# Optimization experiments

Measured on AMD Instinct MI355X. Metric: run time of the kernel, lower is better.

The kernel has to match this reference:

```python
import jax, jax.numpy as jnp
import numpy as np

B, S, D = 4, 2048, 1024
H = 16
HD = D // H  # 64
ROPE_BASE = 10000.0


def _rope_cache(seq_len, dim, dtype=jnp.float32):
    inv_freq = 1.0 / (ROPE_BASE ** (jnp.arange(0, dim, 2, dtype=jnp.float32) / dim))
    t = jnp.arange(seq_len, dtype=jnp.float32)
    freqs = jnp.outer(t, inv_freq)            # [S, dim/2]
    emb = jnp.concatenate([freqs, freqs], -1)  # [S, dim]
    return jnp.cos(emb).astype(dtype), jnp.sin(emb).astype(dtype)


def _rotate_half(x):
    x1, x2 = jnp.split(x, 2, axis=-1)
    return jnp.concatenate([-x2, x1], axis=-1)


def setup_inputs() -> dict:
    key = jax.random.key(0)
    k1, k2, k3 = jax.random.split(key, 3)
    x = jax.random.normal(k1, (B, S, D), dtype=jnp.float32)
    attention_mask = jnp.ones((B, S), dtype=jnp.int32)
    # torch nn.Linear weight is [out, in]; we store [in, out] for x @ W
    w_qkv = jax.random.normal(k2, (D, 3 * D), dtype=jnp.float32) * (1.0 / np.sqrt(D))
    w_out = jax.random.normal(k3, (D, D), dtype=jnp.float32) * (1.0 / np.sqrt(D))
    return {"x": x, "attention_mask": attention_mask, "w_qkv": w_qkv, "w_out": w_out}


def reference(x, attention_mask, w_qkv, w_out):
    b, s, d = x.shape
    qkv = x @ w_qkv                                  # [B,S,3D]
    qkv = qkv.reshape(b, s, 3, H, HD)
    q, k, v = [jnp.transpose(qkv[:, :, i], (0, 2, 1, 3)) for i in range(3)]  # [B,H,S,HD]
    cos, sin = _rope_cache(s, HD, x.dtype)           # [S,HD]
    cos = cos[None, None]                            # [1,1,S,HD]
    sin = sin[None, None]
    q = q * cos + _rotate_half(q) * sin
    k = k * cos + _rotate_half(k) * sin
    scale = 1.0 / np.sqrt(HD)
    scores = jnp.einsum("bhqd,bhkd->bhqk", q, k) * scale  # [B,H,S,S]
    causal = jnp.triu(jnp.ones((s, s), dtype=bool), k=1)
    neg_inf = jnp.finfo(scores.dtype).min
    scores = jnp.where(causal[None, None], -jnp.inf, scores)
    pad = (attention_mask == 0)[:, None, None, :]    # [B,1,1,S]
    scores = jnp.where(pad, -jnp.inf, scores)
    attn = jax.nn.softmax(scores, axis=-1)
    out = jnp.einsum("bhqk,bhkd->bhqd", attn, v)     # [B,H,S,HD]
    out = jnp.transpose(out, (0, 2, 1, 3)).reshape(b, s, d)
    return out @ w_out
```

## Files before the change

### kernel.cpp

```cpp
#include <hip/hip_runtime.h>

#define BQ 4
#define SQ 2048
#define DQ 1024
#define HQ 16
#define BHQ 64

typedef __attribute__((ext_vector_type(8))) short short8;
typedef __attribute__((ext_vector_type(4))) float f32x4;
typedef __attribute__((ext_vector_type(16))) float f32x16;
typedef __attribute__((ext_vector_type(2))) unsigned int u32x2;
typedef unsigned short u16;
typedef unsigned int u32;
typedef unsigned long long u64;

__device__ __forceinline__ u16 f2bf(float f) {
  u32 u = __float_as_uint(f);
  u32 r = u + 0x7fffu + ((u >> 16) & 1u);
  return (u16)(r >> 16);
}
__device__ __forceinline__ float bf2f(u16 h) {
  return __uint_as_float(((u32)h) << 16);
}

__device__ __forceinline__ u32 pkbf(float lo, float hi_) {
  u32 r;
  asm("v_cvt_pk_bf16_f32 %0, %1, %2" : "=v"(r) : "v"(lo), "v"(hi_));
  return r;
}
__device__ __forceinline__ float fexp2(float x) {
  float r;
  asm("v_exp_f32 %0, %1" : "=v"(r) : "v"(x));
  return r;
}
__device__ __forceinline__ float xmax32(float x) { return fmaxf(x, __shfl_xor(x, 32)); }
__device__ __forceinline__ float xsum32(float x) { return x + __shfl_xor(x, 32); }
__device__ __forceinline__ u32 xword(u32 send) { return (u32)__shfl_xor((int)send, 32); }

__device__ __forceinline__ void gload_lds16(const void* g, void* l) {
  __builtin_amdgcn_global_load_lds(
      (const __attribute__((address_space(1))) u32*)(unsigned long long)g,
      (__attribute__((address_space(3))) u32*)(u32)(unsigned long long)l,
      16, 0, 0);
}

__device__ __forceinline__ void transpose_body(const float* __restrict__ in, u16* __restrict__ out,
                                               int R, int C, int bx, int by, int tid) {
  __shared__ float t[32][33];
  int c0 = bx * 32, r0 = by * 32;
  int tx = tid & 31, ty = tid >> 5;
  for (int rr = ty; rr < 32; rr += 8)
    t[rr][tx] = in[(size_t)(r0 + rr) * C + c0 + tx];
  __syncthreads();
  for (int rr = ty; rr < 32; rr += 8)
    out[(size_t)(c0 + rr) * R + r0 + tx] = f2bf(t[tx][rr]);
}

__global__ __launch_bounds__(256) void k_prep(const float* __restrict__ x, u16* __restrict__ xb,
                                              const float* __restrict__ wqkv, u16* __restrict__ wqkvT,
                                              const float* __restrict__ wout, u16* __restrict__ woutT,
                                              float* __restrict__ tab, const int* __restrict__ mask,
                                              u64* __restrict__ mbits) {
  int bid = blockIdx.x, tid = threadIdx.x;
  if (bid < 8192) {
    int i = bid * 256 + tid;
    float4 v = ((const float4*)x)[i];
    ushort4 o;
    o.x = f2bf(v.x); o.y = f2bf(v.y); o.z = f2bf(v.z); o.w = f2bf(v.w);
    ((ushort4*)xb)[i] = o;
  } else if (bid < 11264) {
    int t = bid - 8192;
    transpose_body(wqkv, wqkvT, 1024, 3072, t % 96, t / 96, tid);
  } else if (bid < 12288) {
    int t = bid - 11264;
    transpose_body(wout, woutT, 1024, 1024, t % 32, t / 32, tid);
  } else if (bid < 12544) {
    int i = (bid - 12288) * 256 + tid;
    int s = i >> 5, dp = i & 31;
    float invf = expf(-0.28782313662425576f * (float)dp);
    float ang = (float)s * invf;
    tab[i * 2] = cosf(ang);
    tab[i * 2 + 1] = sinf(ang);
  } else {
    int b = tid >> 6, c = tid & 63;
    int all1 = 1;
    for (int i = 0; i < 32; ++i) all1 &= (mask[b * SQ + c * 32 + i] != 0) ? 1 : 0;
    u64 m = __ballot(all1);
    if (c == 0) mbits[b] = m;
  }
}

template <int EPI>
__global__ __launch_bounds__(256) void k_gemm(const u16* __restrict__ A, const u16* __restrict__ Bt,
                                              float* __restrict__ Cf, u16* __restrict__ qb,
                                              u16* __restrict__ kb, u16* __restrict__ vTs,
                                              const float* __restrict__ tab, int K) {
  __shared__ u16 lA[128 * 64];
  __shared__ u16 lB[128 * 64];
  int bid = blockIdx.x;
  int i_ = bid >> 3;
  int tm = (bid & 7) * 8 + (i_ & 7);
  int tn = i_ >> 3;
  int tid = threadIdx.x, w = tid >> 6, l = tid & 63;
  int wm = w >> 1, wn = w & 1;
  int li = l & 15, lg = l >> 4;
  const u16* gA = A + (size_t)tm * 128 * K;
  const u16* gB = Bt + (size_t)tn * 128 * K;
  f32x4 acc[4][4];
#pragma unroll
  for (int i = 0; i < 4; i++)
#pragma unroll
    for (int j = 0; j < 4; j++) acc[i][j] = (f32x4){0.f, 0.f, 0.f, 0.f};

  int lr = l >> 3, lslot = l & 7;
  int scol = ((lslot ^ lr) * 8);

  for (int kt = 0; kt < K; kt += 64) {
    __syncthreads();
#pragma unroll
    for (int i = 0; i < 4; ++i) {
      int ch = i * 4 + w;
      int row = ch * 8 + lr;
      gload_lds16(gA + (size_t)row * K + kt + scol, &lA[ch * 512]);
      gload_lds16(gB + (size_t)row * K + kt + scol, &lB[ch * 512]);
    }
    __syncthreads();
#pragma unroll
    for (int kk = 0; kk < 2; ++kk) {
      short8 af[4], bfr[4];
#pragma unroll
      for (int mf = 0; mf < 4; ++mf) {
        int row = wm * 64 + mf * 16 + li;
        af[mf] = *(const short8*)&lA[row * 64 + (((kk * 4 + lg)) ^ (row & 7)) * 8];
      }
#pragma unroll
      for (int nf = 0; nf < 4; ++nf) {
        int row = wn * 64 + nf * 16 + li;
        bfr[nf] = *(const short8*)&lB[row * 64 + (((kk * 4 + lg)) ^ (row & 7)) * 8];
      }
#pragma unroll
      for (int mf = 0; mf < 4; ++mf)
#pragma unroll
        for (int nf = 0; nf < 4; ++nf)
          acc[mf][nf] = __builtin_amdgcn_mfma_f32_16x16x32_bf16(af[mf], bfr[nf], acc[mf][nf], 0, 0, 0);
    }
  }
  if (EPI == 0) {
#pragma unroll
    for (int mf = 0; mf < 4; ++mf) {
      int mg0 = tm * 128 + wm * 64 + mf * 16 + lg * 4;
#pragma unroll
      for (int nf = 0; nf < 4; ++nf) {
        int ng = tn * 128 + wn * 64 + nf * 16 + li;
#pragma unroll
        for (int r = 0; r < 4; ++r)
          Cf[(size_t)(mg0 + r) * 1024 + ng] = acc[mf][nf][r];
      }
    }
  } else {
    int which = tn >> 3;
    int h = (tn & 7) * 2 + wn;
    int b = tm >> 4;
    if (which < 2) {
      float scale = (which == 0) ? 0.125f * 1.44269504088896f : 1.0f;
      u16* qk0 = qb + (((size_t)b * HQ + h) * SQ << 6);
      u16* kb0 = kb + ((size_t)b * HQ + h) * (64 * 2048);
#pragma unroll
      for (int mf = 0; mf < 4; ++mf) {
#pragma unroll
        for (int r = 0; r < 4; ++r) {
          int s = (tm * 128 + wm * 64 + mf * 16 + lg * 4 + r) & 2047;
#pragma unroll
          for (int nf2 = 0; nf2 < 2; ++nf2) {
            int dp = nf2 * 16 + li;
            float2 cs = *(const float2*)&tab[(s * 32 + dp) * 2];
            float a = acc[mf][nf2][r];
            float bb = acc[mf][nf2 + 2][r];
            float lo = (a * cs.x - bb * cs.y) * scale;
            float hi2 = (bb * cs.x + a * cs.y) * scale;
            if (which == 0) {
              u16* dst = qk0 + ((size_t)s << 6);
              dst[dp] = f2bf(lo);
              dst[dp + 32] = f2bf(hi2);
            } else {
              u16* dst = kb0 + (s >> 5) * 2048 + (s & 31) * 8;
              dst[(dp >> 3) * 256 + (dp & 7)] = f2bf(lo);
              dst[(dp >> 3) * 256 + 1024 + (dp & 7)] = f2bf(hi2);
            }
          }
        }
      }
    } else {
#pragma unroll
      for (int mf = 0; mf < 4; ++mf) {
        int s0 = (tm * 128 + wm * 64 + mf * 16 + lg * 4) & 2047;
        int kt = s0 >> 5, kk0 = s0 & 31;
        size_t tb = (((size_t)(b * HQ + h) * 64 + kt) * 2048) + (kk0 >> 3) * 512 + (kk0 & 7);
#pragma unroll
        for (int nf = 0; nf < 4; ++nf) {
          int d = nf * 16 + li;
          u32 w0 = pkbf(acc[mf][nf][0], acc[mf][nf][1]);
          u32 w1 = pkbf(acc[mf][nf][2], acc[mf][nf][3]);
          *(u32x2*)&vTs[tb + d * 8] = (u32x2){w0, w1};
        }
      }
    }
  }
}

__global__ __launch_bounds__(256) void k_flash12(const u16* __restrict__ Q, const u16* __restrict__ Kb,
                                                 const u16* __restrict__ VTs, const int* __restrict__ mask,
                                                 const u64* __restrict__ mbits, u16* __restrict__ O) {
  __shared__ alignas(16) u16 Kl[2][4096];
  __shared__ alignas(16) u16 Vl[2][4096];
  int bid = blockIdx.x;
  int bh = bid & 63;
  int u = bid >> 6, v = u & 3, k4 = u >> 2;
  int qsup = (k4 == 0) ? v : (k4 == 1) ? 7 - v : (k4 == 2) ? 8 + v : 15 - v;
  int tid = threadIdx.x, w = tid >> 6, l = tid & 63;
  int j = l & 31, hi = l >> 5;
  int myqt = qsup * 4 + w;
  int P = 2 * qsup + 2;
  int b = bh >> 4, h = bh & 15;
  const int* mp = mask + b * SQ + 4 * hi;
  u64 mb = mbits[b];

  const u16* Kg0 = Kb + (size_t)bh * (64 * 2048) + tid * 8;
  const u16* Vg0 = VTs + (size_t)bh * (64 * 2048) + tid * 8;
  u16* KlB = &Kl[0][(size_t)w * 512];
  u16* VlB = &Vl[0][(size_t)w * 512];

  int qbase = myqt * 32;
  const u16* qp = Q + ((size_t)bh * SQ + qbase + j) * 64 + hi * 8;
  short8 qf[4];
#pragma unroll
  for (int kb = 0; kb < 4; ++kb) qf[kb] = *(const short8*)(qp + kb * 16);

  f32x16 o0, o1;
#pragma unroll
  for (int i = 0; i < 16; ++i) { o0[i] = 0.f; o1[i] = 0.f; }
  float mrun = -INFINITY, lrun = 0.f;

  gload_lds16(Kg0, KlB);
  gload_lds16(Kg0 + 2048, KlB + 2048);
  gload_lds16(Vg0, VlB);
  gload_lds16(Vg0 + 2048, VlB + 2048);
  __syncthreads();

  for (int ph = 0; ph < P; ++ph) {
    int cur = ph & 1;
    if (ph + 1 < P) {
      const u16* kg = Kg0 + (size_t)(2 * ph + 2) * 2048;
      const u16* vg = Vg0 + (size_t)(2 * ph + 2) * 2048;
      u16* kd = KlB + (cur ^ 1) * 4096;
      u16* vd = VlB + (cur ^ 1) * 4096;
      gload_lds16(kg, kd);
      gload_lds16(kg + 2048, kd + 2048);
      gload_lds16(vg, vd);
      gload_lds16(vg + 2048, vd + 2048);
    }

#pragma unroll
    for (int sub = 0; sub < 2; ++sub) {
      int kt = 2 * ph + sub;
      if (kt <= myqt) {
        const u16* Kc = &Kl[cur][sub * 2048];
        const u16* Vc = &Vl[cur][sub * 2048];

        short8 kcf[4];
#pragma unroll
        for (int kb = 0; kb < 4; ++kb)
          kcf[kb] = *(const short8*)&Kc[(hi + 2 * kb) * 256 + j * 8];

        f32x16 s;
#pragma unroll
        for (int i = 0; i < 16; ++i) s[i] = 0.f;
        __builtin_amdgcn_s_setprio(1);
#pragma unroll
        for (int kb = 0; kb < 4; ++kb)
          s = __builtin_amdgcn_mfma_f32_32x32x16_bf16(kcf[kb], qf[kb], s, 0, 0, 0);
        __builtin_amdgcn_s_setprio(0);

        short8 va0 = *(const short8*)&Vc[hi * 512 + j * 8];
        short8 va1 = *(const short8*)&Vc[(hi + 2) * 512 + j * 8];
        short8 vb0 = *(const short8*)&Vc[hi * 512 + (j + 32) * 8];
        short8 vb1 = *(const short8*)&Vc[(hi + 2) * 512 + (j + 32) * 8];

        if (!((mb >> kt) & 1ull)) {
#pragma unroll
          for (int rq = 0; rq < 4; ++rq) {
            int4 mv = *(const int4*)(mp + kt * 32 + 8 * rq);
            if (!mv.x) s[4 * rq + 0] = -INFINITY;
            if (!mv.y) s[4 * rq + 1] = -INFINITY;
            if (!mv.z) s[4 * rq + 2] = -INFINITY;
            if (!mv.w) s[4 * rq + 3] = -INFINITY;
          }
        }
        if (kt == myqt) {
#pragma unroll
          for (int rq = 0; rq < 4; ++rq)
#pragma unroll
            for (int t = 0; t < 4; ++t)
              if (8 * rq + 4 * hi + t > j) s[4 * rq + t] = -INFINITY;
        }

        float t0 = fmaxf(fmaxf(fmaxf(s[0], s[1]), fmaxf(s[2], s[3])),
                         fmaxf(fmaxf(s[4], s[5]), fmaxf(s[6], s[7])));
        t0 = fmaxf(t0, fmaxf(fmaxf(fmaxf(s[8], s[9]), fmaxf(s[10], s[11])),
                             fmaxf(fmaxf(s[12], s[13]), fmaxf(s[14], s[15]))));
        if (!__all(t0 <= mrun + 8.0f)) {
          float tm2 = xmax32(t0);
          float mn = fmaxf(fmaxf(mrun, tm2), -1e30f);
          float alpha = fexp2(mrun - mn);
          mrun = mn;
          lrun *= alpha;
#pragma unroll
          for (int i = 0; i < 16; ++i) { o0[i] *= alpha; o1[i] *= alpha; }
        }
        float ts = 0.f;
#pragma unroll
        for (int i = 0; i < 16; ++i) {
          float pv = fexp2(s[i] - mrun);
          s[i] = pv;
          ts += pv;
        }
        lrun += ts;

        u32 pa[4], pb[4];
#pragma unroll
        for (int q2 = 0; q2 < 4; ++q2) {
          pa[q2] = pkbf(s[4 * q2 + 0], s[4 * q2 + 1]);
          pb[q2] = pkbf(s[4 * q2 + 2], s[4 * q2 + 3]);
        }
        u32 ya01 = xword(hi ? pa[0] : pa[1]);
        u32 yb01 = xword(hi ? pb[0] : pb[1]);
        u32 ya23 = xword(hi ? pa[2] : pa[3]);
        u32 yb23 = xword(hi ? pb[2] : pb[3]);
        union { short8 s8; u32 wd[4]; } f0, f1;
        f0.wd[0] = hi ? ya01 : pa[0];
        f0.wd[1] = hi ? yb01 : pb[0];
        f0.wd[2] = hi ? pa[1] : ya01;
        f0.wd[3] = hi ? pb[1] : yb01;
        f1.wd[0] = hi ? ya23 : pa[2];
        f1.wd[1] = hi ? yb23 : pb[2];
        f1.wd[2] = hi ? pa[3] : ya23;
        f1.wd[3] = hi ? pb[3] : yb23;

        __builtin_amdgcn_s_setprio(1);
        o0 = __builtin_amdgcn_mfma_f32_32x32x16_bf16(va0, f0.s8, o0, 0, 0, 0);
        o0 = __builtin_amdgcn_mfma_f32_32x32x16_bf16(va1, f1.s8, o0, 0, 0, 0);
        o1 = __builtin_amdgcn_mfma_f32_32x32x16_bf16(vb0, f0.s8, o1, 0, 0, 0);
        o1 = __builtin_amdgcn_mfma_f32_32x32x16_bf16(vb1, f1.s8, o1, 0, 0, 0);
        __builtin_amdgcn_s_setprio(0);
      }
    }

    __syncthreads();
  }

  float lfull = xsum32(lrun);
  float inv = 1.0f / lfull;
  u16* ob = O + ((size_t)b * SQ + qbase + j) * DQ + h * 64 + 4 * hi;
#pragma unroll
  for (int q2 = 0; q2 < 4; ++q2) {
#pragma unroll
    for (int e = 0; e < 2; ++e) {
      *(u32*)(ob + 8 * q2 + 2 * e) = pkbf(o0[4 * q2 + 2 * e] * inv, o0[4 * q2 + 2 * e + 1] * inv);
      *(u32*)(ob + 32 + 8 * q2 + 2 * e) = pkbf(o1[4 * q2 + 2 * e] * inv, o1[4 * q2 + 2 * e + 1] * inv);
    }
  }
}

extern "C" void kernel_launch(void* const* d_in, const int* in_sizes, int n_in,
                              void* d_out, int out_size, void* d_ws, size_t ws_size,
                              hipStream_t stream) {
  const float* x = (const float*)d_in[0];
  const int* mask = (const int*)d_in[1];
  const float* wqkv = (const float*)d_in[2];
  const float* wout = (const float*)d_in[3];
  float* out = (float*)d_out;
  char* ws = (char*)d_ws;

  u16* xb    = (u16*)(ws + 0);
  u16* wqkvT = (u16*)(ws + 16777216);
  u16* woutT = (u16*)(ws + 23068672);
  u16* qbuf  = (u16*)(ws + 25165824);
  u16* kbuf  = (u16*)(ws + 41943040);
  u16* vTs   = (u16*)(ws + 75497472);
  u16* attnb = (u16*)(ws + 92274688);
  float* tab = (float*)(ws + 109051904);
  u64* mbits = (u64*)(ws + 109576192);

  k_prep<<<12545, 256, 0, stream>>>(x, xb, wqkv, wqkvT, wout, woutT, tab, mask, mbits);
  k_gemm<1><<<1536, 256, 0, stream>>>(xb, wqkvT, nullptr, qbuf, kbuf, vTs, tab, 1024);
  k_flash12<<<1024, 256, 0, stream>>>(qbuf, kbuf, vTs, mask, mbits, attnb);
  k_gemm<0><<<512, 256, 0, stream>>>(attnb, woutT, out, nullptr, nullptr, nullptr, nullptr, 1024);
}
```

Measured before the change: 185.6 us.

## Split QKV GEMM: 256x256 triple-buffered kernel for Q/K, old kernel for V

```diff
diff --git a/kernel.cpp b/kernel.cpp
--- a/kernel.cpp
+++ b/kernel.cpp
@@ -90,17 +90,125 @@
   }
 }
 
+__global__ __launch_bounds__(512, 2) void k_gemm8(const u16* __restrict__ A, const u16* __restrict__ Bt,
+                                                  u16* __restrict__ qb, u16* __restrict__ kb,
+                                                  const float* __restrict__ tab) {
+  __shared__ u16 ldsA[3][8192];
+  __shared__ u16 ldsB[3][8192];
+  int bid = blockIdx.x;
+  int tn = bid & 7, tm = bid >> 3;
+  int tid = threadIdx.x, w = tid >> 6, l = tid & 63;
+  int wm = w >> 2, wn = w & 3;
+  int li = l & 15, lg = l >> 4;
+
+  int sl0 = w * 64 + l, sl1 = sl0 + 512;
+  const u16* aS0 = A + (size_t)(tm * 256 + (sl0 >> 2)) * 1024 + (sl0 & 3) * 8;
+  const u16* aS1 = A + (size_t)(tm * 256 + (sl1 >> 2)) * 1024 + (sl1 & 3) * 8;
+  const u16* bS0 = Bt + (size_t)(tn * 256 + (sl0 >> 2)) * 1024 + (sl0 & 3) * 8;
+  const u16* bS1 = Bt + (size_t)(tn * 256 + (sl1 >> 2)) * 1024 + (sl1 & 3) * 8;
+
+  f32x4 acc[8][4];
+#pragma unroll
+  for (int i = 0; i < 8; ++i)
+#pragma unroll
+    for (int j = 0; j < 4; ++j) acc[i][j] = (f32x4){0.f, 0.f, 0.f, 0.f};
+
+  gload_lds16(aS0, &ldsA[0][w * 512]);
+  gload_lds16(aS1, &ldsA[0][w * 512 + 4096]);
+  gload_lds16(bS0, &ldsB[0][w * 512]);
+  gload_lds16(bS1, &ldsB[0][w * 512 + 4096]);
+  gload_lds16(aS0 + 32, &ldsA[1][w * 512]);
+  gload_lds16(aS1 + 32, &ldsA[1][w * 512 + 4096]);
+  gload_lds16(bS0 + 32, &ldsB[1][w * 512]);
+  gload_lds16(bS1 + 32, &ldsB[1][w * 512 + 4096]);
+
+  int s = 0;
+  for (int t = 0; t < 32; ++t) {
+    int s2 = s + 2; if (s2 >= 3) s2 -= 3;
+    int tst = (t + 2 < 32) ? t + 2 : 31;
+    asm volatile("s_waitcnt vmcnt(4)" ::: "memory");
+    __builtin_amdgcn_s_barrier();
+    gload_lds16(aS0 + tst * 32, &ldsA[s2][w * 512]);
+    gload_lds16(aS1 + tst * 32, &ldsA[s2][w * 512 + 4096]);
+
+    const u16* As = ldsA[s];
+    const u16* Bs = ldsB[s];
+    short8 bf[4], af[4];
+#pragma unroll
+    for (int nf = 0; nf < 4; ++nf) bf[nf] = *(const short8*)&Bs[(wn * 64 + nf * 16 + li) * 32 + lg * 8];
+#pragma unroll
+    for (int m2 = 0; m2 < 4; ++m2) af[m2] = *(const short8*)&As[(wm * 128 + m2 * 16 + li) * 32 + lg * 8];
+    asm volatile("s_waitcnt lgkmcnt(0)" ::: "memory");
+    __builtin_amdgcn_sched_barrier(0);
+    __builtin_amdgcn_s_setprio(1);
+#pragma unroll
+    for (int m2 = 0; m2 < 4; ++m2)
+#pragma unroll
+      for (int nf = 0; nf < 4; ++nf)
+        acc[m2][nf] = __builtin_amdgcn_mfma_f32_16x16x32_bf16(af[m2], bf[nf], acc[m2][nf], 0, 0, 0);
+    __builtin_amdgcn_s_setprio(0);
+
+    __builtin_amdgcn_s_barrier();
+    gload_lds16(bS0 + tst * 32, &ldsB[s2][w * 512]);
+    gload_lds16(bS1 + tst * 32, &ldsB[s2][w * 512 + 4096]);
+
+#pragma unroll
+    for (int m2 = 0; m2 < 4; ++m2) af[m2] = *(const short8*)&As[(wm * 128 + 64 + m2 * 16 + li) * 32 + lg * 8];
+    asm volatile("s_waitcnt lgkmcnt(0)" ::: "memory");
+    __builtin_amdgcn_sched_barrier(0);
+    __builtin_amdgcn_s_setprio(1);
+#pragma unroll
+    for (int m2 = 0; m2 < 4; ++m2)
+#pragma unroll
+      for (int nf = 0; nf < 4; ++nf)
+        acc[4 + m2][nf] = __builtin_amdgcn_mfma_f32_16x16x32_bf16(af[m2], bf[nf], acc[4 + m2][nf], 0, 0, 0);
+    __builtin_amdgcn_s_setprio(0);
+
+    s = (s == 2) ? 0 : s + 1;
+  }
+
+  int ngb = tn * 256 + wn * 64;
+  int which = ngb >> 10;
+  int h = (ngb >> 6) & 15;
+  float scale = (which == 0) ? 0.125f * 1.44269504088896f : 1.0f;
+#pragma unroll
+  for (int mf = 0; mf < 8; ++mf) {
+#pragma unroll
+    for (int r = 0; r < 4; ++r) {
+      int mg = tm * 256 + wm * 128 + mf * 16 + lg * 4 + r;
+      int b = mg >> 11, sidx = mg & 2047;
+#pragma unroll
+      for (int nf2 = 0; nf2 < 2; ++nf2) {
+        int dp = nf2 * 16 + li;
+        float2 cs = *(const float2*)&tab[(sidx * 32 + dp) * 2];
+        float a = acc[mf][nf2][r];
+        float bb = acc[mf][nf2 + 2][r];
+        float lo = (a * cs.x - bb * cs.y) * scale;
+        float hi2 = (bb * cs.x + a * cs.y) * scale;
+        if (which == 0) {
+          u16* dst = qb + ((((size_t)b * HQ + h) * SQ + sidx) << 6);
+          dst[dp] = f2bf(lo);
+          dst[dp + 32] = f2bf(hi2);
+        } else {
+          u16* dst = kb + ((size_t)b * HQ + h) * (64 * 2048) + (sidx >> 5) * 2048 + (sidx & 31) * 8;
+          dst[(dp >> 3) * 256 + (dp & 7)] = f2bf(lo);
+          dst[(dp >> 3) * 256 + 1024 + (dp & 7)] = f2bf(hi2);
+        }
+      }
+    }
+  }
+}
+
 template <int EPI>
 __global__ __launch_bounds__(256) void k_gemm(const u16* __restrict__ A, const u16* __restrict__ Bt,
-                                              float* __restrict__ Cf, u16* __restrict__ qb,
-                                              u16* __restrict__ kb, u16* __restrict__ vTs,
-                                              const float* __restrict__ tab, int K) {
+                                              float* __restrict__ Cf, u16* __restrict__ vTs,
+                                              int K, int tnoff) {
   __shared__ u16 lA[128 * 64];
   __shared__ u16 lB[128 * 64];
   int bid = blockIdx.x;
   int i_ = bid >> 3;
   int tm = (bid & 7) * 8 + (i_ & 7);
-  int tn = i_ >> 3;
+  int tn = (i_ >> 3) + tnoff;
   int tid = threadIdx.x, w = tid >> 6, l = tid & 63;
   int wm = w >> 1, wn = w & 1;
   int li = l & 15, lg = l >> 4;
@@ -158,51 +266,19 @@
       }
     }
   } else {
-    int which = tn >> 3;
     int h = (tn & 7) * 2 + wn;
     int b = tm >> 4;
-    if (which < 2) {
-      float scale = (which == 0) ? 0.125f * 1.44269504088896f : 1.0f;
-      u16* qk0 = qb + (((size_t)b * HQ + h) * SQ << 6);
-      u16* kb0 = kb + ((size_t)b * HQ + h) * (64 * 2048);
-#pragma unroll
-      for (int mf = 0; mf < 4; ++mf) {
-#pragma unroll
-        for (int r = 0; r < 4; ++r) {
-          int s = (tm * 128 + wm * 64 + mf * 16 + lg * 4 + r) & 2047;
-#pragma unroll
-          for (int nf2 = 0; nf2 < 2; ++nf2) {
-            int dp = nf2 * 16 + li;
-            float2 cs = *(const float2*)&tab[(s * 32 + dp) * 2];
-            float a = acc[mf][nf2][r];
-            float bb = acc[mf][nf2 + 2][r];
-            float lo = (a * cs.x - bb * cs.y) * scale;
-            float hi2 = (bb * cs.x + a * cs.y) * scale;
-            if (which == 0) {
-              u16* dst = qk0 + ((size_t)s << 6);
-              dst[dp] = f2bf(lo);
-              dst[dp + 32] = f2bf(hi2);
-            } else {
-              u16* dst = kb0 + (s >> 5) * 2048 + (s & 31) * 8;
-              dst[(dp >> 3) * 256 + (dp & 7)] = f2bf(lo);
-              dst[(dp >> 3) * 256 + 1024 + (dp & 7)] = f2bf(hi2);
-            }
-          }
-        }
-      }
-    } else {
-#pragma unroll
-      for (int mf = 0; mf < 4; ++mf) {
-        int s0 = (tm * 128 + wm * 64 + mf * 16 + lg * 4) & 2047;
-        int kt = s0 >> 5, kk0 = s0 & 31;
-        size_t tb = (((size_t)(b * HQ + h) * 64 + kt) * 2048) + (kk0 >> 3) * 512 + (kk0 & 7);
-#pragma unroll
-        for (int nf = 0; nf < 4; ++nf) {
-          int d = nf * 16 + li;
-          u32 w0 = pkbf(acc[mf][nf][0], acc[mf][nf][1]);
-          u32 w1 = pkbf(acc[mf][nf][2], acc[mf][nf][3]);
-          *(u32x2*)&vTs[tb + d * 8] = (u32x2){w0, w1};
-        }
+#pragma unroll
+    for (int mf = 0; mf < 4; ++mf) {
+      int s0 = (tm * 128 + wm * 64 + mf * 16 + lg * 4) & 2047;
+      int kt = s0 >> 5, kk0 = s0 & 31;
+      size_t tb = (((size_t)(b * HQ + h) * 64 + kt) * 2048) + (kk0 >> 3) * 512 + (kk0 & 7);
+#pragma unroll
+      for (int nf = 0; nf < 4; ++nf) {
+        int d = nf * 16 + li;
+        u32 w0 = pkbf(acc[mf][nf][0], acc[mf][nf][1]);
+        u32 w1 = pkbf(acc[mf][nf][2], acc[mf][nf][3]);
+        *(u32x2*)&vTs[tb + d * 8] = (u32x2){w0, w1};
       }
     }
   }
@@ -392,7 +468,8 @@
   u64* mbits = (u64*)(ws + 109576192);
 
   k_prep<<<12545, 256, 0, stream>>>(x, xb, wqkv, wqkvT, wout, woutT, tab, mask, mbits);
-  k_gemm<1><<<1536, 256, 0, stream>>>(xb, wqkvT, nullptr, qbuf, kbuf, vTs, tab, 1024);
+  k_gemm8<<<256, 512, 0, stream>>>(xb, wqkvT, qbuf, kbuf, tab);
+  k_gemm<1><<<512, 256, 0, stream>>>(xb, wqkvT, nullptr, vTs, 1024, 16);
   k_flash12<<<1024, 256, 0, stream>>>(qbuf, kbuf, vTs, mask, mbits, attnb);
-  k_gemm<0><<<512, 256, 0, stream>>>(attnb, woutT, out, nullptr, nullptr, nullptr, nullptr, 1024);
-}
+  k_gemm<0><<<512, 256, 0, stream>>>(attnb, woutT, out, nullptr, 1024, 0);
+}
```

Result: slower. 189.4 us (+2.0%).
